# Performance work log

Hardware: AMD Instinct MI355X
Metric: run time of the kernel (lower is better)

## Reference

```python
import jax, jax.numpy as jnp
import numpy as np

N, D_IN, D_H, K, E = 100000, 128, 256, 16, 3200000


def setup_inputs() -> dict:
    key = jax.random.key(0)
    ks = jax.random.split(key, 6)
    x = jax.random.normal(ks[0], (N, D_IN), dtype=jnp.float32)
    edge_index = jax.random.randint(ks[1], (2, E), 0, N, dtype=jnp.int64)
    # Linear params (stored as [in, out] for x @ W + b)
    W1 = jax.random.normal(ks[2], (D_IN, D_H), dtype=jnp.float32) * 0.05
    b1 = jnp.zeros((D_H,), dtype=jnp.float32)
    W2 = jax.random.normal(ks[3], (D_H, K), dtype=jnp.float32) * 0.05
    b2 = jnp.zeros((K,), dtype=jnp.float32)
    return {"x": x, "edge_index": edge_index, "W1": W1, "b1": b1, "W2": W2, "b2": b2}


def reference(x, edge_index, W1, b1, W2, b2):
    # 2-layer MLP + row softmax -> soft cluster assignments C [N, K]
    h = jax.nn.relu(x @ W1 + b1)
    C = jax.nn.softmax(h @ W2 + b2, axis=1)
    # trace((C C^T)^T @ adj) == sum over edges (u,v) of C[u] . C[v]
    # (exact, incl. duplicate edges, since to_dense_adj scatter-adds 1 per edge)
    src, dst = edge_index[0], edge_index[1]
    edge_sum = jnp.sum(C[src] * C[dst])  # [E, K] gathered dot products, reduced
    num_edges = jnp.asarray(edge_index.shape[1], dtype=C.dtype)  # adj.sum()
    modularity_loss = -edge_sum / num_edges
    return (C, modularity_loss)
```

## Files before the change

### kernel.cpp

```cpp
#include <hip/hip_runtime.h>

#define N_NODES 100000
#define D_INF   128
#define D_HID   256
#define K_CL    16
#define N_EDGES 3200000
#define N_TILES (N_NODES / 16)
#define EDGE_BLOCKS (N_EDGES / 512)

typedef __attribute__((ext_vector_type(8))) __bf16  bf16x8;
typedef __attribute__((ext_vector_type(8))) unsigned short u16x8;
typedef __attribute__((ext_vector_type(4))) float   f32x4;

__device__ __forceinline__ unsigned short f2bf(float f) {
    unsigned int u = __builtin_bit_cast(unsigned int, f);
    u += 0x7fffu + ((u >> 16) & 1u);
    return (unsigned short)(u >> 16);
}
__device__ __forceinline__ float bflo(unsigned int p) {
    return __builtin_bit_cast(float, p << 16);
}
__device__ __forceinline__ float bfhi(unsigned int p) {
    return __builtin_bit_cast(float, p & 0xffff0000u);
}

__global__ void prep_kernel(const float* __restrict__ W1,
                            const float* __restrict__ W2,
                            unsigned short* __restrict__ w1t,
                            unsigned short* __restrict__ w2t)
{
    const int i = blockIdx.x * 256 + threadIdx.x;
    if (i < D_INF * D_HID) {
        const int n = i >> 7, k = i & 127;
        w1t[i] = f2bf(W1[k * D_HID + n]);
    }
    if (i < D_HID * K_CL) {
        const int t = i >> 8, n = i & 255;
        w2t[i] = f2bf(W2[n * K_CL + t]);
    }
}

#define W1S 136
#define CHS 40

__global__ __launch_bounds__(256, 2) void mlp_kernel(
    const float* __restrict__ x, const unsigned short* __restrict__ W1T,
    const float* __restrict__ b1, const unsigned short* __restrict__ W2T,
    const float* __restrict__ b2, float* __restrict__ C,
    unsigned short* __restrict__ Cb)
{
    __shared__ unsigned short w1s[256 * W1S];
    __shared__ unsigned short chbuf[4][2][16 * CHS];
    __shared__ float b1s[D_HID];

    const int tid  = threadIdx.x;
    const int wv   = tid >> 6;
    const int lane = tid & 63;
    const int c    = lane & 15;
    const int q    = lane >> 4;

    #pragma unroll
    for (int it = 0; it < 16; ++it) {
        const int idx = it * 256 + tid;
        const int row = idx >> 4, ch = idx & 15;
        const uint4 v = ((const uint4*)W1T)[idx];
        *(uint4*)&w1s[row * W1S + ch * 8] = v;
    }
    if (tid < D_HID) b1s[tid] = b1[tid];

    bf16x8 w2f[8];
    #pragma unroll
    for (int kc2 = 0; kc2 < 8; ++kc2)
        w2f[kc2] = *(const bf16x8*)(W2T + (size_t)c * D_HID + kc2 * 32 + q * 8);
    const float b2v = b2[c];
    __syncthreads();

    unsigned short* const chA = &chbuf[wv][0][0];
    unsigned short* const chB = &chbuf[wv][1][0];

    const int wid     = blockIdx.x * 4 + wv;
    const int wstride = gridDim.x * 4;

    for (int tile = wid; tile < N_TILES; tile += wstride) {
        const int m0 = tile * 16;

        const float* xrow = x + (size_t)(m0 + c) * D_INF + q * 8;
        bf16x8 afr[4];
        #pragma unroll
        for (int kc = 0; kc < 4; ++kc) {
            const float4 xa = *(const float4*)(xrow + kc * 32);
            const float4 xb = *(const float4*)(xrow + kc * 32 + 4);
            u16x8 af;
            af[0] = f2bf(xa.x); af[1] = f2bf(xa.y); af[2] = f2bf(xa.z); af[3] = f2bf(xa.w);
            af[4] = f2bf(xb.x); af[5] = f2bf(xb.y); af[6] = f2bf(xb.z); af[7] = f2bf(xb.w);
            afr[kc] = __builtin_bit_cast(bf16x8, af);
        }

        f32x4 acc2 = (f32x4){0.f, 0.f, 0.f, 0.f};
        #pragma unroll
        for (int kc2 = 0; kc2 < 8; ++kc2) {
            unsigned short* const cb = (kc2 & 1) ? chB : chA;
            #pragma unroll
            for (int half = 0; half < 2; ++half) {
                const int nt = kc2 * 2 + half;
                f32x4 a1 = (f32x4){0.f, 0.f, 0.f, 0.f};
                #pragma unroll
                for (int kc = 0; kc < 4; ++kc) {
                    const bf16x8 bf =
                        *(const bf16x8*)&w1s[(nt * 16 + c) * W1S + kc * 32 + q * 8];
                    a1 = __builtin_amdgcn_mfma_f32_16x16x32_bf16(afr[kc], bf, a1, 0, 0, 0);
                }
                const float bv = b1s[nt * 16 + c];
                #pragma unroll
                for (int r = 0; r < 4; ++r)
                    cb[(4 * q + r) * CHS + half * 16 + c] =
                        f2bf(fmaxf(a1[r] + bv, 0.f));
            }
            const bf16x8 a2 = *(const bf16x8*)&cb[c * CHS + q * 8];
            acc2 = __builtin_amdgcn_mfma_f32_16x16x32_bf16(a2, w2f[kc2], acc2, 0, 0, 0);
        }

        #pragma unroll
        for (int r = 0; r < 4; ++r) {
            const float l = acc2[r] + b2v;
            float mx = l;
            mx = fmaxf(mx, __shfl_xor(mx, 1));
            mx = fmaxf(mx, __shfl_xor(mx, 2));
            mx = fmaxf(mx, __shfl_xor(mx, 4));
            mx = fmaxf(mx, __shfl_xor(mx, 8));
            const float e = __expf(l - mx);
            float sm = e;
            sm += __shfl_xor(sm, 1);
            sm += __shfl_xor(sm, 2);
            sm += __shfl_xor(sm, 4);
            sm += __shfl_xor(sm, 8);
            const float p = e / sm;
            const size_t o = (size_t)(m0 + 4 * q + r) * K_CL + c;
            C[o]  = p;
            Cb[o] = f2bf(p);
        }
    }
}

__global__ __launch_bounds__(256) void edge_kernel(
    const int* __restrict__ ei, const unsigned short* __restrict__ Cb,
    float* __restrict__ partials)
{
    __shared__ float red[4];
    const int tid  = threadIdx.x;
    const int lane = tid & 63;
    const int wv   = tid >> 6;
    const int base = (blockIdx.x * 4 + wv) * 128;

    const int u0 = ei[base + lane];
    const int u1 = ei[base + 64 + lane];
    const int v0 = ei[N_EDGES + base + lane];
    const int v1 = ei[N_EDGES + base + 64 + lane];

    const int half8 = (lane & 1) * 8;
    const int sl    = lane >> 1;

    float s = 0.f;
    #pragma unroll
    for (int g = 0; g < 4; ++g) {
        const int src = (g & 1) * 32 + sl;
        const int ue  = __shfl((g < 2) ? u0 : u1, src);
        const int ve  = __shfl((g < 2) ? v0 : v1, src);
        const uint4 a = *(const uint4*)(Cb + (size_t)ue * K_CL + half8);
        const uint4 b = *(const uint4*)(Cb + (size_t)ve * K_CL + half8);
        s = fmaf(bflo(a.x), bflo(b.x), s);
        s = fmaf(bfhi(a.x), bfhi(b.x), s);
        s = fmaf(bflo(a.y), bflo(b.y), s);
        s = fmaf(bfhi(a.y), bfhi(b.y), s);
        s = fmaf(bflo(a.z), bflo(b.z), s);
        s = fmaf(bfhi(a.z), bfhi(b.z), s);
        s = fmaf(bflo(a.w), bflo(b.w), s);
        s = fmaf(bfhi(a.w), bfhi(b.w), s);
    }
    s += __shfl_xor(s, 1);
    s += __shfl_xor(s, 2);
    s += __shfl_xor(s, 4);
    s += __shfl_xor(s, 8);
    s += __shfl_xor(s, 16);
    s += __shfl_xor(s, 32);
    if (lane == 0) red[wv] = s;
    __syncthreads();
    if (tid == 0) partials[blockIdx.x] = red[0] + red[1] + red[2] + red[3];
}

__global__ __launch_bounds__(256) void finalize_kernel(
    const float* __restrict__ partials, float* __restrict__ out)
{
    __shared__ float red[4];
    const int tid = threadIdx.x;
    float s = 0.f;
    for (int i = tid; i < EDGE_BLOCKS; i += 256) s += partials[i];
    s += __shfl_xor(s, 1);
    s += __shfl_xor(s, 2);
    s += __shfl_xor(s, 4);
    s += __shfl_xor(s, 8);
    s += __shfl_xor(s, 16);
    s += __shfl_xor(s, 32);
    if ((tid & 63) == 0) red[tid >> 6] = s;
    __syncthreads();
    if (tid == 0)
        out[(size_t)N_NODES * K_CL] =
            -(red[0] + red[1] + red[2] + red[3]) / (float)N_EDGES;
}

extern "C" void kernel_launch(void* const* d_in, const int* in_sizes, int n_in,
                              void* d_out, int out_size, void* d_ws, size_t ws_size,
                              hipStream_t stream) {
    const float* x  = (const float*)d_in[0];
    const int*   ei = (const int*)  d_in[1];
    const float* W1 = (const float*)d_in[2];
    const float* b1 = (const float*)d_in[3];
    const float* W2 = (const float*)d_in[4];
    const float* b2 = (const float*)d_in[5];
    float* out = (float*)d_out;

    unsigned short* w1t      = (unsigned short*)d_ws;
    unsigned short* w2t      = (unsigned short*)((char*)d_ws + 65536);
    unsigned short* Cb       = (unsigned short*)((char*)d_ws + 73760);
    float*          partials = (float*)((char*)d_ws + 3273760);

    prep_kernel<<<128, 256, 0, stream>>>(W1, W2, w1t, w2t);
    mlp_kernel<<<512, 256, 0, stream>>>(x, w1t, b1, w2t, b2, out, Cb);
    edge_kernel<<<EDGE_BLOCKS, 256, 0, stream>>>(ei, Cb, partials);
    finalize_kernel<<<1, 256, 0, stream>>>(partials, out);
}
```

Baseline: 155.2 us.

## Process two 16-row tiles per wave in MLP and double edges per wave

Result: slower. 160.2 us (+3.2%).

```diff
diff --git a/kernel.cpp b/kernel.cpp
--- a/kernel.cpp
+++ b/kernel.cpp
@@ -4,9 +4,9 @@
 #define D_INF   128
 #define D_HID   256
 #define K_CL    16
+#define N_PAIRS 3125
 #define N_EDGES 3200000
-#define N_TILES (N_NODES / 16)
-#define EDGE_BLOCKS (N_EDGES / 512)
+#define EDGE_BLOCKS (N_EDGES / 1024)
 
 typedef __attribute__((ext_vector_type(8))) __bf16  bf16x8;
 typedef __attribute__((ext_vector_type(8))) unsigned short u16x8;
@@ -75,54 +75,67 @@
     const float b2v = b2[c];
     __syncthreads();
 
-    unsigned short* const chA = &chbuf[wv][0][0];
-    unsigned short* const chB = &chbuf[wv][1][0];
-
-    const int wid     = blockIdx.x * 4 + wv;
-    const int wstride = gridDim.x * 4;
-
-    for (int tile = wid; tile < N_TILES; tile += wstride) {
-        const int m0 = tile * 16;
-
-        const float* xrow = x + (size_t)(m0 + c) * D_INF + q * 8;
-        bf16x8 afr[4];
+    const int wid = blockIdx.x * 4 + wv;
+    if (wid >= N_PAIRS) return;
+    const int m0 = wid * 32;
+
+    unsigned short* const cb0 = &chbuf[wv][0][0];
+    unsigned short* const cb1 = &chbuf[wv][1][0];
+
+    const float* xr0 = x + (size_t)(m0 + c) * D_INF + q * 8;
+    const float* xr1 = xr0 + 16 * D_INF;
+    bf16x8 af0[4], af1[4];
+    #pragma unroll
+    for (int kc = 0; kc < 4; ++kc) {
+        float4 a = *(const float4*)(xr0 + kc * 32);
+        float4 b = *(const float4*)(xr0 + kc * 32 + 4);
+        u16x8 t;
+        t[0] = f2bf(a.x); t[1] = f2bf(a.y); t[2] = f2bf(a.z); t[3] = f2bf(a.w);
+        t[4] = f2bf(b.x); t[5] = f2bf(b.y); t[6] = f2bf(b.z); t[7] = f2bf(b.w);
+        af0[kc] = __builtin_bit_cast(bf16x8, t);
+        a = *(const float4*)(xr1 + kc * 32);
+        b = *(const float4*)(xr1 + kc * 32 + 4);
+        t[0] = f2bf(a.x); t[1] = f2bf(a.y); t[2] = f2bf(a.z); t[3] = f2bf(a.w);
+        t[4] = f2bf(b.x); t[5] = f2bf(b.y); t[6] = f2bf(b.z); t[7] = f2bf(b.w);
+        af1[kc] = __builtin_bit_cast(bf16x8, t);
+    }
+
+    f32x4 acc2_0 = (f32x4){0.f, 0.f, 0.f, 0.f};
+    f32x4 acc2_1 = (f32x4){0.f, 0.f, 0.f, 0.f};
+    #pragma unroll
+    for (int kc2 = 0; kc2 < 8; ++kc2) {
         #pragma unroll
-        for (int kc = 0; kc < 4; ++kc) {
-            const float4 xa = *(const float4*)(xrow + kc * 32);
-            const float4 xb = *(const float4*)(xrow + kc * 32 + 4);
-            u16x8 af;
-            af[0] = f2bf(xa.x); af[1] = f2bf(xa.y); af[2] = f2bf(xa.z); af[3] = f2bf(xa.w);
-            af[4] = f2bf(xb.x); af[5] = f2bf(xb.y); af[6] = f2bf(xb.z); af[7] = f2bf(xb.w);
-            afr[kc] = __builtin_bit_cast(bf16x8, af);
+        for (int half = 0; half < 2; ++half) {
+            const int nt = kc2 * 2 + half;
+            f32x4 p0 = (f32x4){0.f, 0.f, 0.f, 0.f};
+            f32x4 p1 = (f32x4){0.f, 0.f, 0.f, 0.f};
+            #pragma unroll
+            for (int kc = 0; kc < 4; ++kc) {
+                const bf16x8 bf =
+                    *(const bf16x8*)&w1s[(nt * 16 + c) * W1S + kc * 32 + q * 8];
+                p0 = __builtin_amdgcn_mfma_f32_16x16x32_bf16(af0[kc], bf, p0, 0, 0, 0);
+                p1 = __builtin_amdgcn_mfma_f32_16x16x32_bf16(af1[kc], bf, p1, 0, 0, 0);
+            }
+            const float bv = b1s[nt * 16 + c];
+            #pragma unroll
+            for (int r = 0; r < 4; ++r) {
+                cb0[(4 * q + r) * CHS + half * 16 + c] = f2bf(fmaxf(p0[r] + bv, 0.f));
+                cb1[(4 * q + r) * CHS + half * 16 + c] = f2bf(fmaxf(p1[r] + bv, 0.f));
+            }
         }
-
-        f32x4 acc2 = (f32x4){0.f, 0.f, 0.f, 0.f};
-        #pragma unroll
-        for (int kc2 = 0; kc2 < 8; ++kc2) {
-            unsigned short* const cb = (kc2 & 1) ? chB : chA;
-            #pragma unroll
-            for (int half = 0; half < 2; ++half) {
-                const int nt = kc2 * 2 + half;
-                f32x4 a1 = (f32x4){0.f, 0.f, 0.f, 0.f};
-                #pragma unroll
-                for (int kc = 0; kc < 4; ++kc) {
-                    const bf16x8 bf =
-                        *(const bf16x8*)&w1s[(nt * 16 + c) * W1S + kc * 32 + q * 8];
-                    a1 = __builtin_amdgcn_mfma_f32_16x16x32_bf16(afr[kc], bf, a1, 0, 0, 0);
-                }
-                const float bv = b1s[nt * 16 + c];
-                #pragma unroll
-                for (int r = 0; r < 4; ++r)
-                    cb[(4 * q + r) * CHS + half * 16 + c] =
-                        f2bf(fmaxf(a1[r] + bv, 0.f));
-            }
-            const bf16x8 a2 = *(const bf16x8*)&cb[c * CHS + q * 8];
-            acc2 = __builtin_amdgcn_mfma_f32_16x16x32_bf16(a2, w2f[kc2], acc2, 0, 0, 0);
-        }
-
+        const bf16x8 a20 = *(const bf16x8*)&cb0[c * CHS + q * 8];
+        const bf16x8 a21 = *(const bf16x8*)&cb1[c * CHS + q * 8];
+        acc2_0 = __builtin_amdgcn_mfma_f32_16x16x32_bf16(a20, w2f[kc2], acc2_0, 0, 0, 0);
+        acc2_1 = __builtin_amdgcn_mfma_f32_16x16x32_bf16(a21, w2f[kc2], acc2_1, 0, 0, 0);
+    }
+
+    #pragma unroll
+    for (int t2 = 0; t2 < 2; ++t2) {
+        const f32x4 a2 = t2 ? acc2_1 : acc2_0;
+        const int mb = m0 + t2 * 16;
         #pragma unroll
         for (int r = 0; r < 4; ++r) {
-            const float l = acc2[r] + b2v;
+            const float l = a2[r] + b2v;
             float mx = l;
             mx = fmaxf(mx, __shfl_xor(mx, 1));
             mx = fmaxf(mx, __shfl_xor(mx, 2));
@@ -135,7 +148,7 @@
             sm += __shfl_xor(sm, 4);
             sm += __shfl_xor(sm, 8);
             const float p = e / sm;
-            const size_t o = (size_t)(m0 + 4 * q + r) * K_CL + c;
+            const size_t o = (size_t)(mb + 4 * q + r) * K_CL + c;
             C[o]  = p;
             Cb[o] = f2bf(p);
         }
@@ -150,22 +163,24 @@
     const int tid  = threadIdx.x;
     const int lane = tid & 63;
     const int wv   = tid >> 6;
-    const int base = (blockIdx.x * 4 + wv) * 128;
-
-    const int u0 = ei[base + lane];
-    const int u1 = ei[base + 64 + lane];
-    const int v0 = ei[N_EDGES + base + lane];
-    const int v1 = ei[N_EDGES + base + 64 + lane];
+    const int base = (blockIdx.x * 4 + wv) * 256;
+
+    int u[4], v[4];
+    #pragma unroll
+    for (int j = 0; j < 4; ++j) {
+        u[j] = ei[base + j * 64 + lane];
+        v[j] = ei[N_EDGES + base + j * 64 + lane];
+    }
 
     const int half8 = (lane & 1) * 8;
     const int sl    = lane >> 1;
 
     float s = 0.f;
     #pragma unroll
-    for (int g = 0; g < 4; ++g) {
+    for (int g = 0; g < 8; ++g) {
         const int src = (g & 1) * 32 + sl;
-        const int ue  = __shfl((g < 2) ? u0 : u1, src);
-        const int ve  = __shfl((g < 2) ? v0 : v1, src);
+        const int ue  = __shfl(u[g >> 1], src);
+        const int ve  = __shfl(v[g >> 1], src);
         const uint4 a = *(const uint4*)(Cb + (size_t)ue * K_CL + half8);
         const uint4 b = *(const uint4*)(Cb + (size_t)ve * K_CL + half8);
         s = fmaf(bflo(a.x), bflo(b.x), s);
@@ -225,7 +240,7 @@
     float*          partials = (float*)((char*)d_ws + 3273760);
 
     prep_kernel<<<128, 256, 0, stream>>>(W1, W2, w1t, w2t);
-    mlp_kernel<<<512, 256, 0, stream>>>(x, w1t, b1, w2t, b2, out, Cb);
+    mlp_kernel<<<(N_PAIRS + 3) / 4, 256, 0, stream>>>(x, w1t, b1, w2t, b2, out, Cb);
     edge_kernel<<<EDGE_BLOCKS, 256, 0, stream>>>(ei, Cb, partials);
     finalize_kernel<<<1, 256, 0, stream>>>(partials, out);
 }
```
